# Performance work log

Hardware: AMD Instinct MI355X
Metric: run time of the kernel (lower is better)

Reference implementation:

```python
import jax, jax.numpy as jnp
import numpy as np
import math

N_AGENTS = 16

def _mlp2(x, W1, b1, W2, b2):
    # tanh on first layer only, matching the torch module
    return jnp.tanh(x @ W1 + b1) @ W2 + b2

def setup_inputs() -> dict:
    key = jax.random.key(0)
    ks = jax.random.split(key, 24)
    B, N, A, IN, D = 2048, N_AGENTS, 32, 128, 128
    NODES = B * N
    s = 0.05
    inp = {
        "obs": jax.random.normal(ks[0], (NODES, IN), jnp.float32),
        "policies": jax.random.uniform(ks[1], (NODES, A), jnp.float32),
        "actions": jax.random.uniform(ks[2], (NODES, A), jnp.float32),
        "weights": jax.random.uniform(ks[3], (1,), jnp.float32),
        "noise": jax.random.normal(ks[4], (NODES, N, A), jnp.float32) * 0.1,
        "Wk1": jax.random.normal(ks[5], (IN, 32), jnp.float32) * s,
        "bk1": jnp.zeros((32,), jnp.float32),
        "Wk2": jax.random.normal(ks[6], (32, D), jnp.float32) * s,
        "bk2": jnp.zeros((D,), jnp.float32),
        "Wq1": jax.random.normal(ks[7], (IN, 32), jnp.float32) * s,
        "bq1": jnp.zeros((32,), jnp.float32),
        "Wq2": jax.random.normal(ks[8], (32, D), jnp.float32) * s,
        "bq2": jnp.zeros((D,), jnp.float32),
        "Wv1": jax.random.normal(ks[9], (IN, 32), jnp.float32) * s,
        "bv1": jnp.zeros((32,), jnp.float32),
        "Wv2": jax.random.normal(ks[10], (32, D), jnp.float32) * s,
        "bv2": jnp.zeros((D,), jnp.float32),
        "Wval": jax.random.normal(ks[11], (D + A, 1), jnp.float32) * s,
        "bval": jnp.zeros((1,), jnp.float32),
    }
    return inp

def reference(obs, policies, actions, weights, noise,
              Wk1, bk1, Wk2, bk2, Wq1, bq1, Wq2, bq2, Wv1, bv1, Wv2, bv2,
              Wval, bval):
    N = N_AGENTS
    NODES, _ = obs.shape
    B = NODES // N
    A = policies.shape[-1]
    D = Wk2.shape[1]

    # ---- SoftAttentionInput: graph soft attention over complete N-agent graphs
    k = _mlp2(obs, Wk1, bk1, Wk2, bk2).reshape(B, N, D)
    q = _mlp2(obs, Wq1, bq1, Wq2, bq2).reshape(B, N, D)
    v = _mlp2(obs, Wv1, bv1, Wv2, bv2).reshape(B, N, D)
    # score for receiver i from sender j: key[j] . query[i]
    scores = jnp.einsum('bjd,bid->bij', k, q) / math.sqrt(D)
    alpha = jax.nn.softmax(scores, axis=-1)               # softmax over senders j
    obs_proc = jnp.einsum('bij,bjd->bid', alpha, v)       # [B,N,D]

    # ---- SoftAttentionWeight: PRD mixing of policies and noisy actions
    pi = policies.reshape(B, N, A)
    act = actions.reshape(B, N, A)
    w = weights                                           # scalar mixing weight, shape (1,)
    # z[b,i,k] = w*act[b,k] + (1-w)*pi[b,k] + noise (mailbox of receiver i)
    z = w * act[:, None, :, :] + (1.0 - w) * pi[:, None, :, :] + noise.reshape(B, N, N, A)
    # place_policies construction: z_final[b,i,j,k] = pi[b,k] if k==j else z[b,i,k];
    # mean over k  =>  (pi[b,j] - z[b,i,j] + sum_k z[b,i,k]) / N
    z_sum = jnp.sum(z, axis=2)                            # [B,N,A]
    z_mix = (pi[:, None, :, :] - z + z_sum[:, :, None, :]) / N  # [B,i,j,A]

    obs_b = jnp.broadcast_to(obs_proc[:, None, :, :], (B, N, N, D))  # [b,i,j] = obs_proc[b,j]
    obs_final = jnp.concatenate([obs_b, z_mix], axis=-1).reshape(B * N, N, D + A)

    # ---- ValueNetwork
    x = obs_final @ Wval + bval                           # [B*N, N, 1]
    weights_preproc = alpha.reshape(B * N, N, 1)
    return x, weights_preproc
```

## Files before the change

### kernel.cpp

```cpp
#include <hip/hip_runtime.h>

typedef __attribute__((ext_vector_type(8))) short bf16x8;
typedef __attribute__((ext_vector_type(4))) float f32x4;

__device__ __forceinline__ unsigned short f2bf(float f){
  union { float f; unsigned int u; } v; v.f = f;
  unsigned int u = v.u;
  return (unsigned short)((u + 0x7FFFu + ((u >> 16) & 1u)) >> 16);
}

__device__ __forceinline__ float fast_tanh(float x){
  x = fminf(15.f, fmaxf(-15.f, x));
  float e = __expf(2.f * x);
  return (e - 1.f) / (e + 1.f);
}

__device__ __forceinline__ float dot128(const float* __restrict__ a,
                                        const float* __restrict__ b){
  float s = 0.f;
  for (int c = 0; c < 128; c += 4){
    float4 x = *(const float4*)(a + c);
    float4 y = *(const float4*)(b + c);
    s += x.x*y.x + x.y*y.y + x.z*y.z + x.w*y.w;
  }
  return s;
}

#define GRPSUM(x) { x += __shfl_xor(x, 1); x += __shfl_xor(x, 2); \
                    x += __shfl_xor(x, 4); x += __shfl_xor(x, 8); }


__global__ __launch_bounds__(256) void kn_kernel(
    const float* __restrict__ policies, const float* __restrict__ actions,
    const float* __restrict__ noise, const float* __restrict__ weights,
    const float* __restrict__ Wval, const float* __restrict__ bval,
    const float* __restrict__ Wk1, const float* __restrict__ Wq1, const float* __restrict__ Wv1,
    const float* __restrict__ Wk2, const float* __restrict__ bk2,
    const float* __restrict__ Wq2, const float* __restrict__ bq2,
    const float* __restrict__ Wv2, const float* __restrict__ bv2,
    float* __restrict__ ws, float* __restrict__ out_x)
{
  const int t = threadIdx.x;

  if ((int)blockIdx.x < 4){
    const int tid2 = blockIdx.x * 256 + t;
    const float rs = 0.08838834764831845f;
    unsigned short* bp = (unsigned short*)ws;
    unsigned short* b2 = (unsigned short*)(ws + 6144);

    for (int d = tid2; d < 1602; d += 1024){
      if (d < 1536){
        const int e = d & 7, l = (d >> 3) & 63, tt = d >> 9;
        const int g = (l >> 4) * 8 + e;
        float val = 0.f;
        if (tt < 2){
          const int h = (l & 15) + tt * 16;
          val = rs * dot128(Wk2 + h * 128, Wq2 + g * 128);
        } else if ((l & 15) == 0){
          val = rs * dot128(Wq2 + g * 128, bk2);
        }
        b2[d] = f2bf(val);
      } else if (d < 1600){
        const int h = d - 1536;
        if (h < 32) ws[6912 + h] = rs * dot128(Wk2 + h * 128, bq2);
        else        ws[6944 + (h - 32)] = dot128(Wv2 + (h - 32) * 128, Wval);
      } else if (d == 1600){
        ws[6976] = rs * dot128(bk2, bq2);
      } else {
        ws[6977] = dot128(bv2, Wval);
      }
    }
    for (int idx = tid2; idx < 12288; idx += 1024){
      const int e  = idx & 7;
      const int l  = (idx >> 3) & 63;
      const int kc = (idx >> 9) & 3;
      const int nt = (idx >> 11) & 1;
      const int m  = idx >> 12;
      const float* W1 = (m == 0) ? Wk1 : ((m == 1) ? Wq1 : Wv1);
      const int krow = kc * 32 + (l >> 4) * 8 + e;
      const int col  = nt * 16 + (l & 15);
      bp[idx] = f2bf(W1[krow * 32 + col]);
    }
    return;
  }

  __shared__ __align__(16) float nvw[256];
  __shared__ __align__(16) float pvl[16], avl[16];

  const int b = blockIdx.x - 4;
  const int w = t >> 6, l = t & 63;
  const int q8 = l & 7, r8 = l >> 3;
  const float4 wv4 = *(const float4*)(Wval + 128 + q8 * 4);

  float4 pA0, pA1, aA0, aA1, wpa, wpb;
  const int jp = l >> 2, seg = l & 3;
  if (w == 0){
    const float* pp = policies + (size_t)(b * 16 + jp) * 32 + seg * 8;
    const float* ap = actions  + (size_t)(b * 16 + jp) * 32 + seg * 8;
    pA0 = *(const float4*)(pp);
    pA1 = *(const float4*)(pp + 4);
    aA0 = *(const float4*)(ap);
    aA1 = *(const float4*)(ap + 4);
    wpa = *(const float4*)(Wval + 128 + seg * 8);
    wpb = *(const float4*)(Wval + 132 + seg * 8);
  }

  const float* nbl = noise + (size_t)b * 8192 + (w * 64 + r8) * 32 + q8 * 4;
  float4 nz[8];
#pragma unroll
  for (int p = 0; p < 8; p++) nz[p] = *(const float4*)(nbl + p * 256);
#pragma unroll
  for (int p = 0; p < 8; p++){
    float s = nz[p].x*wv4.x + nz[p].y*wv4.y + nz[p].z*wv4.z + nz[p].w*wv4.w;
    s += __shfl_xor(s, 1); s += __shfl_xor(s, 2); s += __shfl_xor(s, 4);
    if (q8 == 0) nvw[w * 64 + p * 8 + r8] = s;
  }

  if (w == 0){
    float pvv = pA0.x*wpa.x + pA0.y*wpa.y + pA0.z*wpa.z + pA0.w*wpa.w
              + pA1.x*wpb.x + pA1.y*wpb.y + pA1.z*wpb.z + pA1.w*wpb.w;
    float avv = aA0.x*wpa.x + aA0.y*wpa.y + aA0.z*wpa.z + aA0.w*wpa.w
              + aA1.x*wpb.x + aA1.y*wpb.y + aA1.z*wpb.z + aA1.w*wpb.w;
    pvv += __shfl_xor(pvv, 1); pvv += __shfl_xor(pvv, 2);
    avv += __shfl_xor(avv, 1); avv += __shfl_xor(avv, 2);
    if (seg == 0){ pvl[jp] = pvv; avl[jp] = avv; }
  }

  __syncthreads();

  if (w == 0){
    const float wscal = weights[0];
    const float bvs = bval[0];
    const int i = l >> 2, j0 = (l & 3) * 4;
    float4 pv4 = *(const float4*)&pvl[j0];
    float4 av4 = *(const float4*)&avl[j0];
    float4 nv4 = *(const float4*)&nvw[i * 16 + j0];
    const float om = 1.f - wscal;
    float z0 = wscal * av4.x + om * pv4.x + nv4.x;
    float z1 = wscal * av4.y + om * pv4.y + nv4.y;
    float z2 = wscal * av4.z + om * pv4.z + nv4.z;
    float z3 = wscal * av4.w + om * pv4.w + nv4.w;
    float zs = z0 + z1 + z2 + z3;
    zs += __shfl_xor(zs, 1); zs += __shfl_xor(zs, 2);
    float4 o;
    o.x = (pv4.x - z0 + zs) * 0.0625f + bvs;
    o.y = (pv4.y - z1 + zs) * 0.0625f + bvs;
    o.z = (pv4.z - z2 + zs) * 0.0625f + bvs;
    o.w = (pv4.w - z3 + zs) * 0.0625f + bvs;
    *(float4*)(out_x + (size_t)b * 256 + l * 4) = o;
  }
}

__global__ __launch_bounds__(256) void ka_kernel(
    const float* __restrict__ obs,
    const float* __restrict__ bk1p, const float* __restrict__ bq1p, const float* __restrict__ bv1p,
    const float* __restrict__ ws,
    float* __restrict__ out_x, float* __restrict__ out_alpha)
{
  __shared__ __align__(16) unsigned short hk_s[4][512];
  __shared__ __align__(16) unsigned short hq_s[4][512];
  __shared__ __align__(16) unsigned short tq_s[4][512];
  __shared__ __align__(16) float rql_s[4][16];
  __shared__ __align__(16) float vvl_s[4][16];
  __shared__ __align__(16) float ovl_s[4][16];

  const int t = threadIdx.x;
  const int wid = t >> 6, l = t & 63;
  const int b = blockIdx.x * 4 + wid;
  const int li = l & 15, gp = l >> 4;

  const float* orow = obs + (size_t)(b * 16 + li) * 128 + gp * 8;
  float4 ob[8];
#pragma unroll
  for (int kc = 0; kc < 4; kc++){
    ob[kc * 2]     = *(const float4*)(orow + kc * 32);
    ob[kc * 2 + 1] = *(const float4*)(orow + kc * 32 + 4);
  }
  float4 x4 = *(const float4*)(out_x + (size_t)b * 256 + l * 4);

  const bf16x8* bp  = (const bf16x8*)ws;
  const bf16x8* b2p = (const bf16x8*)(ws + 6144);
  const bf16x8 b20 = b2p[l], b21 = b2p[64 + l], b22 = b2p[128 + l];
  const float u0 = ws[6912 + li], u1 = ws[6928 + li];
  const float wv0 = ws[6944 + li], wv1 = ws[6960 + li];
  const float ccv = ws[6976], cvv = ws[6977];
  const float bk0 = bk1p[li], bk1v = bk1p[16 + li];
  const float bq0 = bq1p[li], bq1v = bq1p[16 + li];
  const float bv0 = bv1p[li], bv1v = bv1p[16 + li];

  bf16x8 afr[4];
#pragma unroll
  for (int kc = 0; kc < 4; kc++){
    bf16x8 a;
    a[0]=(short)f2bf(ob[kc*2].x); a[1]=(short)f2bf(ob[kc*2].y);
    a[2]=(short)f2bf(ob[kc*2].z); a[3]=(short)f2bf(ob[kc*2].w);
    a[4]=(short)f2bf(ob[kc*2+1].x); a[5]=(short)f2bf(ob[kc*2+1].y);
    a[6]=(short)f2bf(ob[kc*2+1].z); a[7]=(short)f2bf(ob[kc*2+1].w);
    afr[kc] = a;
  }
  f32x4 acc[6];
#pragma unroll
  for (int mt = 0; mt < 6; mt++){ f32x4 z = {0.f,0.f,0.f,0.f}; acc[mt] = z; }
#pragma unroll
  for (int mt = 0; mt < 6; mt++){
#pragma unroll
    for (int kc = 0; kc < 4; kc++)
      acc[mt] = __builtin_amdgcn_mfma_f32_16x16x32_bf16(afr[kc], bp[(mt*4+kc)*64 + l], acc[mt], 0, 0, 0);
  }

  unsigned short* hkb = hk_s[wid];
  unsigned short* hqb = hq_s[wid];
#pragma unroll
  for (int tile = 0; tile < 2; tile++){
    const float bk_ = tile ? bk1v : bk0;
    const float bq_ = tile ? bq1v : bq0;
    f32x4 ck = acc[tile], cq = acc[2 + tile];
#pragma unroll
    for (int r = 0; r < 4; r++){
      hkb[(gp*4+r)*32 + tile*16 + li] = f2bf(fast_tanh(ck[r] + bk_));
      hqb[(gp*4+r)*32 + tile*16 + li] = f2bf(fast_tanh(cq[r] + bq_));
    }
  }

  {
    f32x4 c0 = acc[4], c1 = acc[5];
    float vp0 = wv0*fast_tanh(c0[0]+bv0) + wv1*fast_tanh(c1[0]+bv1v);
    float vp1 = wv0*fast_tanh(c0[1]+bv0) + wv1*fast_tanh(c1[1]+bv1v);
    float vp2 = wv0*fast_tanh(c0[2]+bv0) + wv1*fast_tanh(c1[2]+bv1v);
    float vp3 = wv0*fast_tanh(c0[3]+bv0) + wv1*fast_tanh(c1[3]+bv1v);
    GRPSUM(vp0); GRPSUM(vp1); GRPSUM(vp2); GRPSUM(vp3);
    if (li == 0){
      float4 vq; vq.x = vp0+cvv; vq.y = vp1+cvv; vq.z = vp2+cvv; vq.w = vp3+cvv;
      *(float4*)&vvl_s[wid][gp*4] = vq;
    }
  }

  const bf16x8 aq = *(const bf16x8*)(hqb + li*32 + gp*8);
  f32x4 cu0 = {u0,u0,u0,u0}, cu1 = {u1,u1,u1,u1}, cu2 = {ccv,ccv,ccv,ccv};
  f32x4 tq0 = __builtin_amdgcn_mfma_f32_16x16x32_bf16(aq, b20, cu0, 0, 0, 0);
  f32x4 tq1 = __builtin_amdgcn_mfma_f32_16x16x32_bf16(aq, b21, cu1, 0, 0, 0);
  f32x4 rqt = __builtin_amdgcn_mfma_f32_16x16x32_bf16(aq, b22, cu2, 0, 0, 0);
  if (li == 0){
    float4 rv; rv.x = rqt[0]; rv.y = rqt[1]; rv.z = rqt[2]; rv.w = rqt[3];
    *(float4*)&rql_s[wid][gp*4] = rv;
  }
  unsigned short* tqb = tq_s[wid];
#pragma unroll
  for (int r = 0; r < 4; r++){
    tqb[(gp*4+r)*32 + li]      = f2bf(tq0[r]);
    tqb[(gp*4+r)*32 + 16 + li] = f2bf(tq1[r]);
  }

  const bf16x8 ak = *(const bf16x8*)(hkb + li*32 + gp*8);
  const bf16x8 bt = *(const bf16x8*)(tqb + li*32 + gp*8);
  f32x4 zz = {0.f,0.f,0.f,0.f};
  f32x4 S = __builtin_amdgcn_mfma_f32_16x16x32_bf16(ak, bt, zz, 0, 0, 0);
  const float rc = rql_s[wid][li];
  float s0 = S[0]+rc, s1 = S[1]+rc, s2 = S[2]+rc, s3 = S[3]+rc;

  float mx = fmaxf(fmaxf(s0, s1), fmaxf(s2, s3));
  mx = fmaxf(mx, __shfl_xor(mx, 16)); mx = fmaxf(mx, __shfl_xor(mx, 32));
  float e0 = __expf(s0-mx), e1 = __expf(s1-mx), e2 = __expf(s2-mx), e3 = __expf(s3-mx);
  float sm = e0+e1+e2+e3;
  sm += __shfl_xor(sm, 16); sm += __shfl_xor(sm, 32);
  const float inv = 1.f / sm;
  const float a0 = e0*inv, a1 = e1*inv, a2 = e2*inv, a3 = e3*inv;

  float* aT = (float*)tqb;
  { float4 av4; av4.x = a0; av4.y = a1; av4.z = a2; av4.w = a3;
    *(float4*)&aT[li*16 + gp*4] = av4; }
  { float4 o4 = *(const float4*)&aT[l*4];
    *(float4*)(out_alpha + (size_t)b*256 + l*4) = o4; }

  float4 vq4 = *(const float4*)&vvl_s[wid][gp*4];
  float ovp = a0*vq4.x + a1*vq4.y + a2*vq4.z + a3*vq4.w;
  ovp += __shfl_xor(ovp, 16); ovp += __shfl_xor(ovp, 32);
  if (l < 16) ovl_s[wid][l] = ovp;

  {
    float4 ov4 = *(const float4*)&ovl_s[wid][(l & 3) * 4];
    x4.x += ov4.x; x4.y += ov4.y; x4.z += ov4.z; x4.w += ov4.w;
    *(float4*)(out_x + (size_t)b * 256 + l * 4) = x4;
  }
}

extern "C" void kernel_launch(void* const* d_in, const int* in_sizes, int n_in,
                              void* d_out, int out_size, void* d_ws, size_t ws_size,
                              hipStream_t stream)
{
  const float* obs      = (const float*)d_in[0];
  const float* policies = (const float*)d_in[1];
  const float* actions  = (const float*)d_in[2];
  const float* weights  = (const float*)d_in[3];
  const float* noise    = (const float*)d_in[4];
  const float* Wk1  = (const float*)d_in[5];
  const float* bk1  = (const float*)d_in[6];
  const float* Wk2  = (const float*)d_in[7];
  const float* bk2  = (const float*)d_in[8];
  const float* Wq1  = (const float*)d_in[9];
  const float* bq1  = (const float*)d_in[10];
  const float* Wq2  = (const float*)d_in[11];
  const float* bq2  = (const float*)d_in[12];
  const float* Wv1  = (const float*)d_in[13];
  const float* bv1  = (const float*)d_in[14];
  const float* Wv2  = (const float*)d_in[15];
  const float* bv2  = (const float*)d_in[16];
  const float* Wval = (const float*)d_in[17];
  const float* bval = (const float*)d_in[18];

  float* out = (float*)d_out;
  float* ws  = (float*)d_ws;

  const int NODES = in_sizes[0] / 128;
  const int B = NODES / 16;

  float* out_x     = out;
  float* out_alpha = out + (size_t)NODES * 16;

  hipLaunchKernelGGL(kn_kernel, dim3(B + 4), dim3(256), 0, stream,
                     policies, actions, noise, weights, Wval, bval,
                     Wk1, Wq1, Wv1, Wk2, bk2, Wq2, bq2, Wv2, bv2,
                     ws, out_x);
  hipLaunchKernelGGL(ka_kernel, dim3(B / 4), dim3(256), 0, stream,
                     obs, bk1, bq1, bv1, ws, out_x, out_alpha);
}
```

Baseline: 29.22 us.

## Split weight prep into tiny kernel and fuse attention and noise paths via atomics

Weight preprocessing moves into a small 64-block kernel that also zero-fills out_x. The noise/policy value path and the attention path then run as different block ranges of one combined launch, each adding its part into out_x with atomicAdd. This removes the dependency where the attention kernel had to read the noise kernel's out_x, so the two memory-heavy stages can overlap. The cost is an extra zero-fill pass over out_x and scalar float atomics in place of vector stores, and the summation order becomes nondeterministic.

```diff
diff --git a/kernel.cpp b/kernel.cpp
--- a/kernel.cpp
+++ b/kernel.cpp
@@ -30,257 +30,264 @@
                     x += __shfl_xor(x, 4); x += __shfl_xor(x, 8); }
 
 
-__global__ __launch_bounds__(256) void kn_kernel(
-    const float* __restrict__ policies, const float* __restrict__ actions,
-    const float* __restrict__ noise, const float* __restrict__ weights,
-    const float* __restrict__ Wval, const float* __restrict__ bval,
+__global__ __launch_bounds__(64) void k0_kernel(
     const float* __restrict__ Wk1, const float* __restrict__ Wq1, const float* __restrict__ Wv1,
     const float* __restrict__ Wk2, const float* __restrict__ bk2,
     const float* __restrict__ Wq2, const float* __restrict__ bq2,
     const float* __restrict__ Wv2, const float* __restrict__ bv2,
-    float* __restrict__ ws, float* __restrict__ out_x)
+    const float* __restrict__ Wval, float* __restrict__ ws,
+    float* __restrict__ out_x, int nx4)
+{
+  const int tid = blockIdx.x * 64 + threadIdx.x;
+  const float rs = 0.08838834764831845f;
+  unsigned short* bp = (unsigned short*)ws;
+  unsigned short* b2 = (unsigned short*)(ws + 6144);
+
+  if (tid < 1536){
+    const int e = tid & 7, l = (tid >> 3) & 63, tt = tid >> 9;
+    const int g = (l >> 4) * 8 + e;
+    float val = 0.f;
+    if (tt < 2){
+      const int h = (l & 15) + tt * 16;
+      val = rs * dot128(Wk2 + h * 128, Wq2 + g * 128);
+    } else if ((l & 15) == 0){
+      val = rs * dot128(Wq2 + g * 128, bk2);
+    }
+    b2[tid] = f2bf(val);
+  } else if (tid < 1600){
+    const int h = tid - 1536;
+    if (h < 32) ws[6912 + h] = rs * dot128(Wk2 + h * 128, bq2);
+    else        ws[6944 + (h - 32)] = dot128(Wv2 + (h - 32) * 128, Wval);
+  } else if (tid == 1600){
+    ws[6976] = rs * dot128(bk2, bq2);
+  } else if (tid == 1601){
+    ws[6977] = dot128(bv2, Wval);
+  }
+
+  for (int idx = tid; idx < 12288; idx += 4096){
+    const int e  = idx & 7;
+    const int l  = (idx >> 3) & 63;
+    const int kc = (idx >> 9) & 3;
+    const int nt = (idx >> 11) & 1;
+    const int m  = idx >> 12;
+    const float* W1 = (m == 0) ? Wk1 : ((m == 1) ? Wq1 : Wv1);
+    const int krow = kc * 32 + (l >> 4) * 8 + e;
+    const int col  = nt * 16 + (l & 15);
+    bp[idx] = f2bf(W1[krow * 32 + col]);
+  }
+
+  float4 z4 = {0.f, 0.f, 0.f, 0.f};
+  float4* ox = (float4*)out_x;
+  for (int i = tid; i < nx4; i += 4096) ox[i] = z4;
+}
+
+__global__ __launch_bounds__(256) void mega_kernel(
+    const float* __restrict__ obs,
+    const float* __restrict__ policies, const float* __restrict__ actions,
+    const float* __restrict__ noise, const float* __restrict__ weights,
+    const float* __restrict__ bk1p, const float* __restrict__ bq1p, const float* __restrict__ bv1p,
+    const float* __restrict__ Wval, const float* __restrict__ bval,
+    const float* __restrict__ ws,
+    float* __restrict__ out_x, float* __restrict__ out_alpha, int BA)
 {
   const int t = threadIdx.x;
-
-  if ((int)blockIdx.x < 4){
-    const int tid2 = blockIdx.x * 256 + t;
-    const float rs = 0.08838834764831845f;
-    unsigned short* bp = (unsigned short*)ws;
-    unsigned short* b2 = (unsigned short*)(ws + 6144);
-
-    for (int d = tid2; d < 1602; d += 1024){
-      if (d < 1536){
-        const int e = d & 7, l = (d >> 3) & 63, tt = d >> 9;
-        const int g = (l >> 4) * 8 + e;
-        float val = 0.f;
-        if (tt < 2){
-          const int h = (l & 15) + tt * 16;
-          val = rs * dot128(Wk2 + h * 128, Wq2 + g * 128);
-        } else if ((l & 15) == 0){
-          val = rs * dot128(Wq2 + g * 128, bk2);
-        }
-        b2[d] = f2bf(val);
-      } else if (d < 1600){
-        const int h = d - 1536;
-        if (h < 32) ws[6912 + h] = rs * dot128(Wk2 + h * 128, bq2);
-        else        ws[6944 + (h - 32)] = dot128(Wv2 + (h - 32) * 128, Wval);
-      } else if (d == 1600){
-        ws[6976] = rs * dot128(bk2, bq2);
-      } else {
-        ws[6977] = dot128(bv2, Wval);
+  const int bid = blockIdx.x;
+
+  if (bid < BA){
+    __shared__ __align__(16) unsigned short hk_s[4][512];
+    __shared__ __align__(16) unsigned short hq_s[4][512];
+    __shared__ __align__(16) unsigned short tq_s[4][512];
+    __shared__ __align__(16) float rql_s[4][16];
+    __shared__ __align__(16) float vvl_s[4][16];
+    __shared__ __align__(16) float ovl_s[4][16];
+
+    const int wid = t >> 6, l = t & 63;
+    const int b = bid * 4 + wid;
+    const int li = l & 15, gp = l >> 4;
+
+    const float* orow = obs + (size_t)(b * 16 + li) * 128 + gp * 8;
+    float4 ob[8];
+#pragma unroll
+    for (int kc = 0; kc < 4; kc++){
+      ob[kc * 2]     = *(const float4*)(orow + kc * 32);
+      ob[kc * 2 + 1] = *(const float4*)(orow + kc * 32 + 4);
+    }
+
+    const bf16x8* bp  = (const bf16x8*)ws;
+    const bf16x8* b2p = (const bf16x8*)(ws + 6144);
+    const bf16x8 b20 = b2p[l], b21 = b2p[64 + l], b22 = b2p[128 + l];
+    const float u0 = ws[6912 + li], u1 = ws[6928 + li];
+    const float wv0 = ws[6944 + li], wv1 = ws[6960 + li];
+    const float ccv = ws[6976], cvv = ws[6977];
+    const float bk0 = bk1p[li], bk1v = bk1p[16 + li];
+    const float bq0 = bq1p[li], bq1v = bq1p[16 + li];
+    const float bv0 = bv1p[li], bv1v = bv1p[16 + li];
+
+    bf16x8 afr[4];
+#pragma unroll
+    for (int kc = 0; kc < 4; kc++){
+      bf16x8 a;
+      a[0]=(short)f2bf(ob[kc*2].x); a[1]=(short)f2bf(ob[kc*2].y);
+      a[2]=(short)f2bf(ob[kc*2].z); a[3]=(short)f2bf(ob[kc*2].w);
+      a[4]=(short)f2bf(ob[kc*2+1].x); a[5]=(short)f2bf(ob[kc*2+1].y);
+      a[6]=(short)f2bf(ob[kc*2+1].z); a[7]=(short)f2bf(ob[kc*2+1].w);
+      afr[kc] = a;
+    }
+    f32x4 acc[6];
+#pragma unroll
+    for (int mt = 0; mt < 6; mt++){ f32x4 z = {0.f,0.f,0.f,0.f}; acc[mt] = z; }
+#pragma unroll
+    for (int mt = 0; mt < 6; mt++){
+#pragma unroll
+      for (int kc = 0; kc < 4; kc++)
+        acc[mt] = __builtin_amdgcn_mfma_f32_16x16x32_bf16(afr[kc], bp[(mt*4+kc)*64 + l], acc[mt], 0, 0, 0);
+    }
+
+    unsigned short* hkb = hk_s[wid];
+    unsigned short* hqb = hq_s[wid];
+#pragma unroll
+    for (int tile = 0; tile < 2; tile++){
+      const float bk_ = tile ? bk1v : bk0;
+      const float bq_ = tile ? bq1v : bq0;
+      f32x4 ck = acc[tile], cq = acc[2 + tile];
+#pragma unroll
+      for (int r = 0; r < 4; r++){
+        hkb[(gp*4+r)*32 + tile*16 + li] = f2bf(fast_tanh(ck[r] + bk_));
+        hqb[(gp*4+r)*32 + tile*16 + li] = f2bf(fast_tanh(cq[r] + bq_));
       }
     }
-    for (int idx = tid2; idx < 12288; idx += 1024){
-      const int e  = idx & 7;
-      const int l  = (idx >> 3) & 63;
-      const int kc = (idx >> 9) & 3;
-      const int nt = (idx >> 11) & 1;
-      const int m  = idx >> 12;
-      const float* W1 = (m == 0) ? Wk1 : ((m == 1) ? Wq1 : Wv1);
-      const int krow = kc * 32 + (l >> 4) * 8 + e;
-      const int col  = nt * 16 + (l & 15);
-      bp[idx] = f2bf(W1[krow * 32 + col]);
+
+    {
+      f32x4 c0 = acc[4], c1 = acc[5];
+      float vp0 = wv0*fast_tanh(c0[0]+bv0) + wv1*fast_tanh(c1[0]+bv1v);
+      float vp1 = wv0*fast_tanh(c0[1]+bv0) + wv1*fast_tanh(c1[1]+bv1v);
+      float vp2 = wv0*fast_tanh(c0[2]+bv0) + wv1*fast_tanh(c1[2]+bv1v);
+      float vp3 = wv0*fast_tanh(c0[3]+bv0) + wv1*fast_tanh(c1[3]+bv1v);
+      GRPSUM(vp0); GRPSUM(vp1); GRPSUM(vp2); GRPSUM(vp3);
+      if (li == 0){
+        float4 vq; vq.x = vp0+cvv; vq.y = vp1+cvv; vq.z = vp2+cvv; vq.w = vp3+cvv;
+        *(float4*)&vvl_s[wid][gp*4] = vq;
+      }
+    }
+
+    const bf16x8 aq = *(const bf16x8*)(hqb + li*32 + gp*8);
+    f32x4 cu0 = {u0,u0,u0,u0}, cu1 = {u1,u1,u1,u1}, cu2 = {ccv,ccv,ccv,ccv};
+    f32x4 tq0 = __builtin_amdgcn_mfma_f32_16x16x32_bf16(aq, b20, cu0, 0, 0, 0);
+    f32x4 tq1 = __builtin_amdgcn_mfma_f32_16x16x32_bf16(aq, b21, cu1, 0, 0, 0);
+    f32x4 rqt = __builtin_amdgcn_mfma_f32_16x16x32_bf16(aq, b22, cu2, 0, 0, 0);
+    if (li == 0){
+      float4 rv; rv.x = rqt[0]; rv.y = rqt[1]; rv.z = rqt[2]; rv.w = rqt[3];
+      *(float4*)&rql_s[wid][gp*4] = rv;
+    }
+    unsigned short* tqb = tq_s[wid];
+#pragma unroll
+    for (int r = 0; r < 4; r++){
+      tqb[(gp*4+r)*32 + li]      = f2bf(tq0[r]);
+      tqb[(gp*4+r)*32 + 16 + li] = f2bf(tq1[r]);
+    }
+
+    const bf16x8 ak = *(const bf16x8*)(hkb + li*32 + gp*8);
+    const bf16x8 bt = *(const bf16x8*)(tqb + li*32 + gp*8);
+    f32x4 zz = {0.f,0.f,0.f,0.f};
+    f32x4 S = __builtin_amdgcn_mfma_f32_16x16x32_bf16(ak, bt, zz, 0, 0, 0);
+    const float rc = rql_s[wid][li];
+    float s0 = S[0]+rc, s1 = S[1]+rc, s2 = S[2]+rc, s3 = S[3]+rc;
+
+    float mx = fmaxf(fmaxf(s0, s1), fmaxf(s2, s3));
+    mx = fmaxf(mx, __shfl_xor(mx, 16)); mx = fmaxf(mx, __shfl_xor(mx, 32));
+    float e0 = __expf(s0-mx), e1 = __expf(s1-mx), e2 = __expf(s2-mx), e3 = __expf(s3-mx);
+    float sm = e0+e1+e2+e3;
+    sm += __shfl_xor(sm, 16); sm += __shfl_xor(sm, 32);
+    const float inv = 1.f / sm;
+    const float a0 = e0*inv, a1 = e1*inv, a2 = e2*inv, a3 = e3*inv;
+
+    float* aT = (float*)tqb;
+    { float4 av4; av4.x = a0; av4.y = a1; av4.z = a2; av4.w = a3;
+      *(float4*)&aT[li*16 + gp*4] = av4; }
+    { float4 o4 = *(const float4*)&aT[l*4];
+      *(float4*)(out_alpha + (size_t)b*256 + l*4) = o4; }
+
+    float4 vq4 = *(const float4*)&vvl_s[wid][gp*4];
+    float ovp = a0*vq4.x + a1*vq4.y + a2*vq4.z + a3*vq4.w;
+    ovp += __shfl_xor(ovp, 16); ovp += __shfl_xor(ovp, 32);
+    if (l < 16) ovl_s[wid][l] = ovp;
+
+    {
+      float4 ov4 = *(const float4*)&ovl_s[wid][(l & 3) * 4];
+      float* dst = out_x + (size_t)b * 256 + l * 4;
+      atomicAdd(dst + 0, ov4.x);
+      atomicAdd(dst + 1, ov4.y);
+      atomicAdd(dst + 2, ov4.z);
+      atomicAdd(dst + 3, ov4.w);
     }
     return;
   }
 
-  __shared__ __align__(16) float nvw[256];
-  __shared__ __align__(16) float pvl[16], avl[16];
-
-  const int b = blockIdx.x - 4;
-  const int w = t >> 6, l = t & 63;
-  const int q8 = l & 7, r8 = l >> 3;
-  const float4 wv4 = *(const float4*)(Wval + 128 + q8 * 4);
-
-  float4 pA0, pA1, aA0, aA1, wpa, wpb;
-  const int jp = l >> 2, seg = l & 3;
-  if (w == 0){
-    const float* pp = policies + (size_t)(b * 16 + jp) * 32 + seg * 8;
-    const float* ap = actions  + (size_t)(b * 16 + jp) * 32 + seg * 8;
-    pA0 = *(const float4*)(pp);
-    pA1 = *(const float4*)(pp + 4);
-    aA0 = *(const float4*)(ap);
-    aA1 = *(const float4*)(ap + 4);
-    wpa = *(const float4*)(Wval + 128 + seg * 8);
-    wpb = *(const float4*)(Wval + 132 + seg * 8);
-  }
-
-  const float* nbl = noise + (size_t)b * 8192 + (w * 64 + r8) * 32 + q8 * 4;
-  float4 nz[8];
-#pragma unroll
-  for (int p = 0; p < 8; p++) nz[p] = *(const float4*)(nbl + p * 256);
-#pragma unroll
-  for (int p = 0; p < 8; p++){
-    float s = nz[p].x*wv4.x + nz[p].y*wv4.y + nz[p].z*wv4.z + nz[p].w*wv4.w;
-    s += __shfl_xor(s, 1); s += __shfl_xor(s, 2); s += __shfl_xor(s, 4);
-    if (q8 == 0) nvw[w * 64 + p * 8 + r8] = s;
-  }
-
-  if (w == 0){
-    float pvv = pA0.x*wpa.x + pA0.y*wpa.y + pA0.z*wpa.z + pA0.w*wpa.w
-              + pA1.x*wpb.x + pA1.y*wpb.y + pA1.z*wpb.z + pA1.w*wpb.w;
-    float avv = aA0.x*wpa.x + aA0.y*wpa.y + aA0.z*wpa.z + aA0.w*wpa.w
-              + aA1.x*wpb.x + aA1.y*wpb.y + aA1.z*wpb.z + aA1.w*wpb.w;
-    pvv += __shfl_xor(pvv, 1); pvv += __shfl_xor(pvv, 2);
-    avv += __shfl_xor(avv, 1); avv += __shfl_xor(avv, 2);
-    if (seg == 0){ pvl[jp] = pvv; avl[jp] = avv; }
-  }
-
-  __syncthreads();
-
-  if (w == 0){
-    const float wscal = weights[0];
-    const float bvs = bval[0];
-    const int i = l >> 2, j0 = (l & 3) * 4;
-    float4 pv4 = *(const float4*)&pvl[j0];
-    float4 av4 = *(const float4*)&avl[j0];
-    float4 nv4 = *(const float4*)&nvw[i * 16 + j0];
-    const float om = 1.f - wscal;
-    float z0 = wscal * av4.x + om * pv4.x + nv4.x;
-    float z1 = wscal * av4.y + om * pv4.y + nv4.y;
-    float z2 = wscal * av4.z + om * pv4.z + nv4.z;
-    float z3 = wscal * av4.w + om * pv4.w + nv4.w;
-    float zs = z0 + z1 + z2 + z3;
-    zs += __shfl_xor(zs, 1); zs += __shfl_xor(zs, 2);
-    float4 o;
-    o.x = (pv4.x - z0 + zs) * 0.0625f + bvs;
-    o.y = (pv4.y - z1 + zs) * 0.0625f + bvs;
-    o.z = (pv4.z - z2 + zs) * 0.0625f + bvs;
-    o.w = (pv4.w - z3 + zs) * 0.0625f + bvs;
-    *(float4*)(out_x + (size_t)b * 256 + l * 4) = o;
-  }
-}
-
-__global__ __launch_bounds__(256) void ka_kernel(
-    const float* __restrict__ obs,
-    const float* __restrict__ bk1p, const float* __restrict__ bq1p, const float* __restrict__ bv1p,
-    const float* __restrict__ ws,
-    float* __restrict__ out_x, float* __restrict__ out_alpha)
-{
-  __shared__ __align__(16) unsigned short hk_s[4][512];
-  __shared__ __align__(16) unsigned short hq_s[4][512];
-  __shared__ __align__(16) unsigned short tq_s[4][512];
-  __shared__ __align__(16) float rql_s[4][16];
-  __shared__ __align__(16) float vvl_s[4][16];
-  __shared__ __align__(16) float ovl_s[4][16];
-
-  const int t = threadIdx.x;
-  const int wid = t >> 6, l = t & 63;
-  const int b = blockIdx.x * 4 + wid;
-  const int li = l & 15, gp = l >> 4;
-
-  const float* orow = obs + (size_t)(b * 16 + li) * 128 + gp * 8;
-  float4 ob[8];
-#pragma unroll
-  for (int kc = 0; kc < 4; kc++){
-    ob[kc * 2]     = *(const float4*)(orow + kc * 32);
-    ob[kc * 2 + 1] = *(const float4*)(orow + kc * 32 + 4);
-  }
-  float4 x4 = *(const float4*)(out_x + (size_t)b * 256 + l * 4);
-
-  const bf16x8* bp  = (const bf16x8*)ws;
-  const bf16x8* b2p = (const bf16x8*)(ws + 6144);
-  const bf16x8 b20 = b2p[l], b21 = b2p[64 + l], b22 = b2p[128 + l];
-  const float u0 = ws[6912 + li], u1 = ws[6928 + li];
-  const float wv0 = ws[6944 + li], wv1 = ws[6960 + li];
-  const float ccv = ws[6976], cvv = ws[6977];
-  const float bk0 = bk1p[li], bk1v = bk1p[16 + li];
-  const float bq0 = bq1p[li], bq1v = bq1p[16 + li];
-  const float bv0 = bv1p[li], bv1v = bv1p[16 + li];
-
-  bf16x8 afr[4];
-#pragma unroll
-  for (int kc = 0; kc < 4; kc++){
-    bf16x8 a;
-    a[0]=(short)f2bf(ob[kc*2].x); a[1]=(short)f2bf(ob[kc*2].y);
-    a[2]=(short)f2bf(ob[kc*2].z); a[3]=(short)f2bf(ob[kc*2].w);
-    a[4]=(short)f2bf(ob[kc*2+1].x); a[5]=(short)f2bf(ob[kc*2+1].y);
-    a[6]=(short)f2bf(ob[kc*2+1].z); a[7]=(short)f2bf(ob[kc*2+1].w);
-    afr[kc] = a;
-  }
-  f32x4 acc[6];
-#pragma unroll
-  for (int mt = 0; mt < 6; mt++){ f32x4 z = {0.f,0.f,0.f,0.f}; acc[mt] = z; }
-#pragma unroll
-  for (int mt = 0; mt < 6; mt++){
-#pragma unroll
-    for (int kc = 0; kc < 4; kc++)
-      acc[mt] = __builtin_amdgcn_mfma_f32_16x16x32_bf16(afr[kc], bp[(mt*4+kc)*64 + l], acc[mt], 0, 0, 0);
-  }
-
-  unsigned short* hkb = hk_s[wid];
-  unsigned short* hqb = hq_s[wid];
-#pragma unroll
-  for (int tile = 0; tile < 2; tile++){
-    const float bk_ = tile ? bk1v : bk0;
-    const float bq_ = tile ? bq1v : bq0;
-    f32x4 ck = acc[tile], cq = acc[2 + tile];
-#pragma unroll
-    for (int r = 0; r < 4; r++){
-      hkb[(gp*4+r)*32 + tile*16 + li] = f2bf(fast_tanh(ck[r] + bk_));
-      hqb[(gp*4+r)*32 + tile*16 + li] = f2bf(fast_tanh(cq[r] + bq_));
-    }
-  }
-
   {
-    f32x4 c0 = acc[4], c1 = acc[5];
-    float vp0 = wv0*fast_tanh(c0[0]+bv0) + wv1*fast_tanh(c1[0]+bv1v);
-    float vp1 = wv0*fast_tanh(c0[1]+bv0) + wv1*fast_tanh(c1[1]+bv1v);
-    float vp2 = wv0*fast_tanh(c0[2]+bv0) + wv1*fast_tanh(c1[2]+bv1v);
-    float vp3 = wv0*fast_tanh(c0[3]+bv0) + wv1*fast_tanh(c1[3]+bv1v);
-    GRPSUM(vp0); GRPSUM(vp1); GRPSUM(vp2); GRPSUM(vp3);
-    if (li == 0){
-      float4 vq; vq.x = vp0+cvv; vq.y = vp1+cvv; vq.z = vp2+cvv; vq.w = vp3+cvv;
-      *(float4*)&vvl_s[wid][gp*4] = vq;
-    }
-  }
-
-  const bf16x8 aq = *(const bf16x8*)(hqb + li*32 + gp*8);
-  f32x4 cu0 = {u0,u0,u0,u0}, cu1 = {u1,u1,u1,u1}, cu2 = {ccv,ccv,ccv,ccv};
-  f32x4 tq0 = __builtin_amdgcn_mfma_f32_16x16x32_bf16(aq, b20, cu0, 0, 0, 0);
-  f32x4 tq1 = __builtin_amdgcn_mfma_f32_16x16x32_bf16(aq, b21, cu1, 0, 0, 0);
-  f32x4 rqt = __builtin_amdgcn_mfma_f32_16x16x32_bf16(aq, b22, cu2, 0, 0, 0);
-  if (li == 0){
-    float4 rv; rv.x = rqt[0]; rv.y = rqt[1]; rv.z = rqt[2]; rv.w = rqt[3];
-    *(float4*)&rql_s[wid][gp*4] = rv;
-  }
-  unsigned short* tqb = tq_s[wid];
-#pragma unroll
-  for (int r = 0; r < 4; r++){
-    tqb[(gp*4+r)*32 + li]      = f2bf(tq0[r]);
-    tqb[(gp*4+r)*32 + 16 + li] = f2bf(tq1[r]);
-  }
-
-  const bf16x8 ak = *(const bf16x8*)(hkb + li*32 + gp*8);
-  const bf16x8 bt = *(const bf16x8*)(tqb + li*32 + gp*8);
-  f32x4 zz = {0.f,0.f,0.f,0.f};
-  f32x4 S = __builtin_amdgcn_mfma_f32_16x16x32_bf16(ak, bt, zz, 0, 0, 0);
-  const float rc = rql_s[wid][li];
-  float s0 = S[0]+rc, s1 = S[1]+rc, s2 = S[2]+rc, s3 = S[3]+rc;
-
-  float mx = fmaxf(fmaxf(s0, s1), fmaxf(s2, s3));
-  mx = fmaxf(mx, __shfl_xor(mx, 16)); mx = fmaxf(mx, __shfl_xor(mx, 32));
-  float e0 = __expf(s0-mx), e1 = __expf(s1-mx), e2 = __expf(s2-mx), e3 = __expf(s3-mx);
-  float sm = e0+e1+e2+e3;
-  sm += __shfl_xor(sm, 16); sm += __shfl_xor(sm, 32);
-  const float inv = 1.f / sm;
-  const float a0 = e0*inv, a1 = e1*inv, a2 = e2*inv, a3 = e3*inv;
-
-  float* aT = (float*)tqb;
-  { float4 av4; av4.x = a0; av4.y = a1; av4.z = a2; av4.w = a3;
-    *(float4*)&aT[li*16 + gp*4] = av4; }
-  { float4 o4 = *(const float4*)&aT[l*4];
-    *(float4*)(out_alpha + (size_t)b*256 + l*4) = o4; }
-
-  float4 vq4 = *(const float4*)&vvl_s[wid][gp*4];
-  float ovp = a0*vq4.x + a1*vq4.y + a2*vq4.z + a3*vq4.w;
-  ovp += __shfl_xor(ovp, 16); ovp += __shfl_xor(ovp, 32);
-  if (l < 16) ovl_s[wid][l] = ovp;
-
-  {
-    float4 ov4 = *(const float4*)&ovl_s[wid][(l & 3) * 4];
-    x4.x += ov4.x; x4.y += ov4.y; x4.z += ov4.z; x4.w += ov4.w;
-    *(float4*)(out_x + (size_t)b * 256 + l * 4) = x4;
+    __shared__ __align__(16) float nvw[256];
+    __shared__ __align__(16) float pvl[16], avl[16];
+
+    const int b = bid - BA;
+    const int w = t >> 6, l = t & 63;
+    const int q8 = l & 7, r8 = l >> 3;
+    const float4 wv4 = *(const float4*)(Wval + 128 + q8 * 4);
+
+    float4 pA0, pA1, aA0, aA1, wpa, wpb;
+    const int jp = l >> 2, seg = l & 3;
+    if (w == 0){
+      const float* pp = policies + (size_t)(b * 16 + jp) * 32 + seg * 8;
+      const float* ap = actions  + (size_t)(b * 16 + jp) * 32 + seg * 8;
+      pA0 = *(const float4*)(pp);
+      pA1 = *(const float4*)(pp + 4);
+      aA0 = *(const float4*)(ap);
+      aA1 = *(const float4*)(ap + 4);
+      wpa = *(const float4*)(Wval + 128 + seg * 8);
+      wpb = *(const float4*)(Wval + 132 + seg * 8);
+    }
+
+    const float* nbl = noise + (size_t)b * 8192 + (w * 64 + r8) * 32 + q8 * 4;
+    float4 nz[8];
+#pragma unroll
+    for (int p = 0; p < 8; p++) nz[p] = *(const float4*)(nbl + p * 256);
+#pragma unroll
+    for (int p = 0; p < 8; p++){
+      float s = nz[p].x*wv4.x + nz[p].y*wv4.y + nz[p].z*wv4.z + nz[p].w*wv4.w;
+      s += __shfl_xor(s, 1); s += __shfl_xor(s, 2); s += __shfl_xor(s, 4);
+      if (q8 == 0) nvw[w * 64 + p * 8 + r8] = s;
+    }
+
+    if (w == 0){
+      float pvv = pA0.x*wpa.x + pA0.y*wpa.y + pA0.z*wpa.z + pA0.w*wpa.w
+                + pA1.x*wpb.x + pA1.y*wpb.y + pA1.z*wpb.z + pA1.w*wpb.w;
+      float avv = aA0.x*wpa.x + aA0.y*wpa.y + aA0.z*wpa.z + aA0.w*wpa.w
+                + aA1.x*wpb.x + aA1.y*wpb.y + aA1.z*wpb.z + aA1.w*wpb.w;
+      pvv += __shfl_xor(pvv, 1); pvv += __shfl_xor(pvv, 2);
+      avv += __shfl_xor(avv, 1); avv += __shfl_xor(avv, 2);
+      if (seg == 0){ pvl[jp] = pvv; avl[jp] = avv; }
+    }
+
+    __syncthreads();
+
+    if (w == 0){
+      const float wscal = weights[0];
+      const float bvs = bval[0];
+      const int i = l >> 2, j0 = (l & 3) * 4;
+      float4 pv4 = *(const float4*)&pvl[j0];
+      float4 av4 = *(const float4*)&avl[j0];
+      float4 nv4 = *(const float4*)&nvw[i * 16 + j0];
+      const float om = 1.f - wscal;
+      float z0 = wscal * av4.x + om * pv4.x + nv4.x;
+      float z1 = wscal * av4.y + om * pv4.y + nv4.y;
+      float z2 = wscal * av4.z + om * pv4.z + nv4.z;
+      float z3 = wscal * av4.w + om * pv4.w + nv4.w;
+      float zs = z0 + z1 + z2 + z3;
+      zs += __shfl_xor(zs, 1); zs += __shfl_xor(zs, 2);
+      float* dst = out_x + (size_t)b * 256 + l * 4;
+      atomicAdd(dst + 0, (pv4.x - z0 + zs) * 0.0625f + bvs);
+      atomicAdd(dst + 1, (pv4.y - z1 + zs) * 0.0625f + bvs);
+      atomicAdd(dst + 2, (pv4.z - z2 + zs) * 0.0625f + bvs);
+      atomicAdd(dst + 3, (pv4.w - z3 + zs) * 0.0625f + bvs);
+    }
   }
 }
 
@@ -313,14 +320,16 @@
 
   const int NODES = in_sizes[0] / 128;
   const int B = NODES / 16;
+  const int BA = B / 4;
 
   float* out_x     = out;
   float* out_alpha = out + (size_t)NODES * 16;
 
-  hipLaunchKernelGGL(kn_kernel, dim3(B + 4), dim3(256), 0, stream,
-                     policies, actions, noise, weights, Wval, bval,
-                     Wk1, Wq1, Wv1, Wk2, bk2, Wq2, bq2, Wv2, bv2,
-                     ws, out_x);
-  hipLaunchKernelGGL(ka_kernel, dim3(B / 4), dim3(256), 0, stream,
-                     obs, bk1, bq1, bv1, ws, out_x, out_alpha);
-}
+  hipLaunchKernelGGL(k0_kernel, dim3(64), dim3(64), 0, stream,
+                     Wk1, Wq1, Wv1, Wk2, bk2, Wq2, bq2, Wv2, bv2, Wval, ws,
+                     out_x, NODES * 16 / 4);
+  hipLaunchKernelGGL(mega_kernel, dim3(BA + B), dim3(256), 0, stream,
+                     obs, policies, actions, noise, weights,
+                     bk1, bq1, bv1, Wval, bval, ws,
+                     out_x, out_alpha, BA);
+}
```

Measured after the change: 36.69 us. +25.6%, slower.

## Recompute packed weights per block in LDS and reorder kernels to drop out_x round-trip

Applied to the files above, without the earlier changes.

Weight preprocessing moves out of kn_kernel's 4 dedicated blocks. It includes the Wk2·Wq2 products, the bias folds and the bf16 packing of the first-layer weights. Every attention block now recomputes them redundantly into shared memory, and the MFMA B-fragments are read from LDS. The launch order is swapped: ka_kernel runs first and writes only the attention-value term to the workspace, then kn_kernel combines it with the mixing term and writes out_x once. This removes the serial dependency on a few prep blocks and the read-modify-write of out_x. The cost is a large amount of duplicated dot-product and packing work in every block, plus extra LDS use.

```diff
diff --git a/kernel.cpp b/kernel.cpp
--- a/kernel.cpp
+++ b/kernel.cpp
@@ -29,145 +29,30 @@
 #define GRPSUM(x) { x += __shfl_xor(x, 1); x += __shfl_xor(x, 2); \
                     x += __shfl_xor(x, 4); x += __shfl_xor(x, 8); }
 
-
-__global__ __launch_bounds__(256) void kn_kernel(
-    const float* __restrict__ policies, const float* __restrict__ actions,
-    const float* __restrict__ noise, const float* __restrict__ weights,
-    const float* __restrict__ Wval, const float* __restrict__ bval,
+__global__ __launch_bounds__(256) void ka_kernel(
+    const float* __restrict__ obs,
     const float* __restrict__ Wk1, const float* __restrict__ Wq1, const float* __restrict__ Wv1,
     const float* __restrict__ Wk2, const float* __restrict__ bk2,
     const float* __restrict__ Wq2, const float* __restrict__ bq2,
     const float* __restrict__ Wv2, const float* __restrict__ bv2,
-    float* __restrict__ ws, float* __restrict__ out_x)
+    const float* __restrict__ Wval,
+    const float* __restrict__ bk1p, const float* __restrict__ bq1p, const float* __restrict__ bv1p,
+    float* __restrict__ out_alpha, float* __restrict__ ws_ov)
 {
-  const int t = threadIdx.x;
-
-  if ((int)blockIdx.x < 4){
-    const int tid2 = blockIdx.x * 256 + t;
-    const float rs = 0.08838834764831845f;
-    unsigned short* bp = (unsigned short*)ws;
-    unsigned short* b2 = (unsigned short*)(ws + 6144);
-
-    for (int d = tid2; d < 1602; d += 1024){
-      if (d < 1536){
-        const int e = d & 7, l = (d >> 3) & 63, tt = d >> 9;
-        const int g = (l >> 4) * 8 + e;
-        float val = 0.f;
-        if (tt < 2){
-          const int h = (l & 15) + tt * 16;
-          val = rs * dot128(Wk2 + h * 128, Wq2 + g * 128);
-        } else if ((l & 15) == 0){
-          val = rs * dot128(Wq2 + g * 128, bk2);
-        }
-        b2[d] = f2bf(val);
-      } else if (d < 1600){
-        const int h = d - 1536;
-        if (h < 32) ws[6912 + h] = rs * dot128(Wk2 + h * 128, bq2);
-        else        ws[6944 + (h - 32)] = dot128(Wv2 + (h - 32) * 128, Wval);
-      } else if (d == 1600){
-        ws[6976] = rs * dot128(bk2, bq2);
-      } else {
-        ws[6977] = dot128(bv2, Wval);
-      }
-    }
-    for (int idx = tid2; idx < 12288; idx += 1024){
-      const int e  = idx & 7;
-      const int l  = (idx >> 3) & 63;
-      const int kc = (idx >> 9) & 3;
-      const int nt = (idx >> 11) & 1;
-      const int m  = idx >> 12;
-      const float* W1 = (m == 0) ? Wk1 : ((m == 1) ? Wq1 : Wv1);
-      const int krow = kc * 32 + (l >> 4) * 8 + e;
-      const int col  = nt * 16 + (l & 15);
-      bp[idx] = f2bf(W1[krow * 32 + col]);
-    }
-    return;
-  }
-
-  __shared__ __align__(16) float nvw[256];
-  __shared__ __align__(16) float pvl[16], avl[16];
-
-  const int b = blockIdx.x - 4;
-  const int w = t >> 6, l = t & 63;
-  const int q8 = l & 7, r8 = l >> 3;
-  const float4 wv4 = *(const float4*)(Wval + 128 + q8 * 4);
-
-  float4 pA0, pA1, aA0, aA1, wpa, wpb;
-  const int jp = l >> 2, seg = l & 3;
-  if (w == 0){
-    const float* pp = policies + (size_t)(b * 16 + jp) * 32 + seg * 8;
-    const float* ap = actions  + (size_t)(b * 16 + jp) * 32 + seg * 8;
-    pA0 = *(const float4*)(pp);
-    pA1 = *(const float4*)(pp + 4);
-    aA0 = *(const float4*)(ap);
-    aA1 = *(const float4*)(ap + 4);
-    wpa = *(const float4*)(Wval + 128 + seg * 8);
-    wpb = *(const float4*)(Wval + 132 + seg * 8);
-  }
-
-  const float* nbl = noise + (size_t)b * 8192 + (w * 64 + r8) * 32 + q8 * 4;
-  float4 nz[8];
-#pragma unroll
-  for (int p = 0; p < 8; p++) nz[p] = *(const float4*)(nbl + p * 256);
-#pragma unroll
-  for (int p = 0; p < 8; p++){
-    float s = nz[p].x*wv4.x + nz[p].y*wv4.y + nz[p].z*wv4.z + nz[p].w*wv4.w;
-    s += __shfl_xor(s, 1); s += __shfl_xor(s, 2); s += __shfl_xor(s, 4);
-    if (q8 == 0) nvw[w * 64 + p * 8 + r8] = s;
-  }
-
-  if (w == 0){
-    float pvv = pA0.x*wpa.x + pA0.y*wpa.y + pA0.z*wpa.z + pA0.w*wpa.w
-              + pA1.x*wpb.x + pA1.y*wpb.y + pA1.z*wpb.z + pA1.w*wpb.w;
-    float avv = aA0.x*wpa.x + aA0.y*wpa.y + aA0.z*wpa.z + aA0.w*wpa.w
-              + aA1.x*wpb.x + aA1.y*wpb.y + aA1.z*wpb.z + aA1.w*wpb.w;
-    pvv += __shfl_xor(pvv, 1); pvv += __shfl_xor(pvv, 2);
-    avv += __shfl_xor(avv, 1); avv += __shfl_xor(avv, 2);
-    if (seg == 0){ pvl[jp] = pvv; avl[jp] = avv; }
-  }
-
-  __syncthreads();
-
-  if (w == 0){
-    const float wscal = weights[0];
-    const float bvs = bval[0];
-    const int i = l >> 2, j0 = (l & 3) * 4;
-    float4 pv4 = *(const float4*)&pvl[j0];
-    float4 av4 = *(const float4*)&avl[j0];
-    float4 nv4 = *(const float4*)&nvw[i * 16 + j0];
-    const float om = 1.f - wscal;
-    float z0 = wscal * av4.x + om * pv4.x + nv4.x;
-    float z1 = wscal * av4.y + om * pv4.y + nv4.y;
-    float z2 = wscal * av4.z + om * pv4.z + nv4.z;
-    float z3 = wscal * av4.w + om * pv4.w + nv4.w;
-    float zs = z0 + z1 + z2 + z3;
-    zs += __shfl_xor(zs, 1); zs += __shfl_xor(zs, 2);
-    float4 o;
-    o.x = (pv4.x - z0 + zs) * 0.0625f + bvs;
-    o.y = (pv4.y - z1 + zs) * 0.0625f + bvs;
-    o.z = (pv4.z - z2 + zs) * 0.0625f + bvs;
-    o.w = (pv4.w - z3 + zs) * 0.0625f + bvs;
-    *(float4*)(out_x + (size_t)b * 256 + l * 4) = o;
-  }
-}
-
-__global__ __launch_bounds__(256) void ka_kernel(
-    const float* __restrict__ obs,
-    const float* __restrict__ bk1p, const float* __restrict__ bq1p, const float* __restrict__ bv1p,
-    const float* __restrict__ ws,
-    float* __restrict__ out_x, float* __restrict__ out_alpha)
-{
+  __shared__ __align__(16) unsigned short bpack_s[12288];
+  __shared__ __align__(16) unsigned short b2_s[1536];
+  __shared__ __align__(16) float u_s[32], wv_s[32], cc_s[2];
   __shared__ __align__(16) unsigned short hk_s[4][512];
   __shared__ __align__(16) unsigned short hq_s[4][512];
   __shared__ __align__(16) unsigned short tq_s[4][512];
   __shared__ __align__(16) float rql_s[4][16];
   __shared__ __align__(16) float vvl_s[4][16];
-  __shared__ __align__(16) float ovl_s[4][16];
 
   const int t = threadIdx.x;
   const int wid = t >> 6, l = t & 63;
   const int b = blockIdx.x * 4 + wid;
   const int li = l & 15, gp = l >> 4;
+  const float rs = 0.08838834764831845f;
 
   const float* orow = obs + (size_t)(b * 16 + li) * 128 + gp * 8;
   float4 ob[8];
@@ -176,14 +61,41 @@
     ob[kc * 2]     = *(const float4*)(orow + kc * 32);
     ob[kc * 2 + 1] = *(const float4*)(orow + kc * 32 + 4);
   }
-  float4 x4 = *(const float4*)(out_x + (size_t)b * 256 + l * 4);
-
-  const bf16x8* bp  = (const bf16x8*)ws;
-  const bf16x8* b2p = (const bf16x8*)(ws + 6144);
-  const bf16x8 b20 = b2p[l], b21 = b2p[64 + l], b22 = b2p[128 + l];
-  const float u0 = ws[6912 + li], u1 = ws[6928 + li];
-  const float wv0 = ws[6944 + li], wv1 = ws[6960 + li];
-  const float ccv = ws[6976], cvv = ws[6977];
+
+  for (int i = t; i < 512; i += 256)
+    if ((i >> 3) & 15) b2_s[1024 + i] = 0;
+  for (int idx = t; idx < 1024; idx += 256){
+    const int h = idx & 31, g = idx >> 5;
+    const float val = rs * dot128(Wk2 + h * 128, Wq2 + g * 128);
+    b2_s[(h >> 4) * 512 + ((((g >> 3) << 4) | (h & 15)) << 3) + (g & 7)] = f2bf(val);
+  }
+  for (int g = t; g < 32; g += 256){
+    const float val = rs * dot128(Wq2 + g * 128, bk2);
+    b2_s[1024 + (g >> 3) * 128 + (g & 7)] = f2bf(val);
+  }
+  for (int idx = t; idx < 66; idx += 256){
+    if (idx < 32)       u_s[idx]       = rs * dot128(Wk2 + idx * 128, bq2);
+    else if (idx < 64)  wv_s[idx - 32] = dot128(Wv2 + (idx - 32) * 128, Wval);
+    else if (idx == 64) cc_s[0]        = rs * dot128(bk2, bq2);
+    else                cc_s[1]        = dot128(bv2, Wval);
+  }
+  for (int idx = t; idx < 12288; idx += 256){
+    const int e  = idx & 7;
+    const int ll = (idx >> 3) & 63;
+    const int kc = (idx >> 9) & 3;
+    const int nt = (idx >> 11) & 1;
+    const int m  = idx >> 12;
+    const float* W1 = (m == 0) ? Wk1 : ((m == 1) ? Wq1 : Wv1);
+    bpack_s[idx] = f2bf(W1[(kc * 32 + (ll >> 4) * 8 + e) * 32 + nt * 16 + (ll & 15)]);
+  }
+  __syncthreads();
+
+  const bf16x8 b20 = *(const bf16x8*)(b2_s + (size_t)l * 8);
+  const bf16x8 b21 = *(const bf16x8*)(b2_s + 512 + (size_t)l * 8);
+  const bf16x8 b22 = *(const bf16x8*)(b2_s + 1024 + (size_t)l * 8);
+  const float u0 = u_s[li], u1 = u_s[16 + li];
+  const float wv0 = wv_s[li], wv1 = wv_s[16 + li];
+  const float ccv = cc_s[0], cvv = cc_s[1];
   const float bk0 = bk1p[li], bk1v = bk1p[16 + li];
   const float bq0 = bq1p[li], bq1v = bq1p[16 + li];
   const float bv0 = bv1p[li], bv1v = bv1p[16 + li];
@@ -204,8 +116,10 @@
 #pragma unroll
   for (int mt = 0; mt < 6; mt++){
 #pragma unroll
-    for (int kc = 0; kc < 4; kc++)
-      acc[mt] = __builtin_amdgcn_mfma_f32_16x16x32_bf16(afr[kc], bp[(mt*4+kc)*64 + l], acc[mt], 0, 0, 0);
+    for (int kc = 0; kc < 4; kc++){
+      const bf16x8 bfr = *(const bf16x8*)(bpack_s + (size_t)((mt*4+kc)*64 + l) * 8);
+      acc[mt] = __builtin_amdgcn_mfma_f32_16x16x32_bf16(afr[kc], bfr, acc[mt], 0, 0, 0);
+    }
   }
 
   unsigned short* hkb = hk_s[wid];
@@ -275,12 +189,69 @@
   float4 vq4 = *(const float4*)&vvl_s[wid][gp*4];
   float ovp = a0*vq4.x + a1*vq4.y + a2*vq4.z + a3*vq4.w;
   ovp += __shfl_xor(ovp, 16); ovp += __shfl_xor(ovp, 32);
-  if (l < 16) ovl_s[wid][l] = ovp;
+  if (l < 16) ws_ov[(size_t)b*16 + l] = ovp;
+}
+
+__global__ __launch_bounds__(256) void kn_kernel(
+    const float* __restrict__ policies, const float* __restrict__ actions,
+    const float* __restrict__ noise, const float* __restrict__ weights,
+    const float* __restrict__ Wval, const float* __restrict__ bval,
+    const float* __restrict__ ws_ov, float* __restrict__ out_x)
+{
+  __shared__ __align__(16) float nvw[256];
+  __shared__ __align__(16) float pvl[16], avl[16], ovl[16];
+
+  const int b = blockIdx.x, t = threadIdx.x;
+  const int w = t >> 6, l = t & 63;
+  const int q8 = l & 7, r8 = l >> 3;
+  const float4 wv4 = *(const float4*)(Wval + 128 + q8 * 4);
+
+  float4 pA0, pA1, aA0, aA1, wpa, wpb;
+  const int jp = l >> 2, seg = l & 3;
+  if (w == 0){
+    if (t < 16) ovl[t] = ws_ov[(size_t)b * 16 + t];
+    const float* pp = policies + (size_t)(b * 16 + jp) * 32 + seg * 8;
+    const float* ap = actions  + (size_t)(b * 16 + jp) * 32 + seg * 8;
+    pA0 = *(const float4*)(pp);
+    pA1 = *(const float4*)(pp + 4);
+    aA0 = *(const float4*)(ap);
+    aA1 = *(const float4*)(ap + 4);
+    wpa = *(const float4*)(Wval + 128 + seg * 8);
+    wpb = *(const float4*)(Wval + 132 + seg * 8);
+  }
+
+  const float* nbl = noise + (size_t)b * 8192 + (w * 64 + r8) * 32 + q8 * 4;
+  float4 nz[8];
+#pragma unroll
+  for (int p = 0; p < 8; p++) nz[p] = *(const float4*)(nbl + p * 256);
+#pragma unroll
+  for (int p = 0; p < 8; p++){
+    float s = nz[p].x*wv4.x + nz[p].y*wv4.y + nz[p].z*wv4.z + nz[p].w*wv4.w;
+    s += __shfl_xor(s, 1); s += __shfl_xor(s, 2); s += __shfl_xor(s, 4);
+    if (q8 == 0) nvw[w * 64 + p * 8 + r8] = s;
+  }
+
+  if (w == 0){
+    float pvv = pA0.x*wpa.x + pA0.y*wpa.y + pA0.z*wpa.z + pA0.w*wpa.w
+              + pA1.x*wpb.x + pA1.y*wpb.y + pA1.z*wpb.z + pA1.w*wpb.w;
+    float avv = aA0.x*wpa.x + aA0.y*wpa.y + aA0.z*wpa.z + aA0.w*wpa.w
+              + aA1.x*wpb.x + aA1.y*wpb.y + aA1.z*wpb.z + aA1.w*wpb.w;
+    pvv += __shfl_xor(pvv, 1); pvv += __shfl_xor(pvv, 2);
+    avv += __shfl_xor(avv, 1); avv += __shfl_xor(avv, 2);
+    if (seg == 0){ pvl[jp] = pvv; avl[jp] = avv; }
+  }
+
+  __syncthreads();
 
   {
-    float4 ov4 = *(const float4*)&ovl_s[wid][(l & 3) * 4];
-    x4.x += ov4.x; x4.y += ov4.y; x4.z += ov4.z; x4.w += ov4.w;
-    *(float4*)(out_x + (size_t)b * 256 + l * 4) = x4;
+    const float wscal = weights[0];
+    const float bvs = bval[0];
+    const int j = t & 15;
+    const float pv = pvl[j], av = avl[j];
+    const float zval = wscal * av + (1.f - wscal) * pv + nvw[t];
+    float zs = zval;
+    GRPSUM(zs);
+    out_x[(size_t)b * 256 + t] = ovl[j] + (pv - zval + zs) * 0.0625f + bvs;
   }
 }
 
@@ -310,6 +281,7 @@
 
   float* out = (float*)d_out;
   float* ws  = (float*)d_ws;
+  float* ws_ov = ws;
 
   const int NODES = in_sizes[0] / 128;
   const int B = NODES / 16;
@@ -317,10 +289,10 @@
   float* out_x     = out;
   float* out_alpha = out + (size_t)NODES * 16;
 
-  hipLaunchKernelGGL(kn_kernel, dim3(B + 4), dim3(256), 0, stream,
+  hipLaunchKernelGGL(ka_kernel, dim3(B / 4), dim3(256), 0, stream,
+                     obs, Wk1, Wq1, Wv1, Wk2, bk2, Wq2, bq2, Wv2, bv2, Wval,
+                     bk1, bq1, bv1, out_alpha, ws_ov);
+  hipLaunchKernelGGL(kn_kernel, dim3(B), dim3(256), 0, stream,
                      policies, actions, noise, weights, Wval, bval,
-                     Wk1, Wq1, Wv1, Wk2, bk2, Wq2, bq2, Wv2, bv2,
-                     ws, out_x);
-  hipLaunchKernelGGL(ka_kernel, dim3(B / 4), dim3(256), 0, stream,
-                     obs, bk1, bq1, bv1, ws, out_x, out_alpha);
-}
+                     ws_ov, out_x);
+}
```

After: 71.84 us. 146% more time.

## Stage packed bf16 weight table in LDS and software-pipeline MFMA B loads

Applied to the files above, without the earlier changes.

Each block now cooperatively copies the packed bf16 weight table and small float constants from global memory into shared memory, with a block barrier, instead of having every wave read B fragments straight from global. The MFMA loop then double-buffers the B fragments, loading the next tile's four fragments from LDS while issuing the current tile's MFMAs. This targets repeated global/L2 latency on weight loads. In exchange it adds about 27KB of LDS per block, which may lower occupancy, plus a __syncthreads and a copy cost paid by every block.

```diff
diff --git a/kernel.cpp b/kernel.cpp
--- a/kernel.cpp
+++ b/kernel.cpp
@@ -157,6 +157,8 @@
     const float* __restrict__ ws,
     float* __restrict__ out_x, float* __restrict__ out_alpha)
 {
+  __shared__ __align__(16) unsigned short tabu[13824];
+  __shared__ __align__(16) float tabf[68];
   __shared__ __align__(16) unsigned short hk_s[4][512];
   __shared__ __align__(16) unsigned short hq_s[4][512];
   __shared__ __align__(16) unsigned short tq_s[4][512];
@@ -178,12 +180,24 @@
   }
   float4 x4 = *(const float4*)(out_x + (size_t)b * 256 + l * 4);
 
-  const bf16x8* bp  = (const bf16x8*)ws;
-  const bf16x8* b2p = (const bf16x8*)(ws + 6144);
+  {
+    const float4* src = (const float4*)ws;
+    float4* dst = (float4*)tabu;
+#pragma unroll
+    for (int i = 0; i < 7; i++){
+      const int idx = t + i * 256;
+      if (idx < 1728) dst[idx] = src[idx];
+    }
+    if (t < 66) tabf[t] = ws[6912 + t];
+  }
+  __syncthreads();
+
+  const bf16x8* bpl = (const bf16x8*)tabu;
+  const bf16x8* b2p = (const bf16x8*)(tabu + 12288);
   const bf16x8 b20 = b2p[l], b21 = b2p[64 + l], b22 = b2p[128 + l];
-  const float u0 = ws[6912 + li], u1 = ws[6928 + li];
-  const float wv0 = ws[6944 + li], wv1 = ws[6960 + li];
-  const float ccv = ws[6976], cvv = ws[6977];
+  const float u0 = tabf[li], u1 = tabf[16 + li];
+  const float wv0 = tabf[32 + li], wv1 = tabf[48 + li];
+  const float ccv = tabf[64], cvv = tabf[65];
   const float bk0 = bk1p[li], bk1v = bk1p[16 + li];
   const float bq0 = bq1p[li], bq1v = bq1p[16 + li];
   const float bv0 = bv1p[li], bv1v = bv1p[16 + li];
@@ -198,14 +212,23 @@
     a[6]=(short)f2bf(ob[kc*2+1].z); a[7]=(short)f2bf(ob[kc*2+1].w);
     afr[kc] = a;
   }
+
   f32x4 acc[6];
 #pragma unroll
   for (int mt = 0; mt < 6; mt++){ f32x4 z = {0.f,0.f,0.f,0.f}; acc[mt] = z; }
+  bf16x8 cur0 = bpl[l], cur1 = bpl[64 + l], cur2 = bpl[128 + l], cur3 = bpl[192 + l];
 #pragma unroll
   for (int mt = 0; mt < 6; mt++){
-#pragma unroll
-    for (int kc = 0; kc < 4; kc++)
-      acc[mt] = __builtin_amdgcn_mfma_f32_16x16x32_bf16(afr[kc], bp[(mt*4+kc)*64 + l], acc[mt], 0, 0, 0);
+    bf16x8 nxt0, nxt1, nxt2, nxt3;
+    if (mt < 5){
+      const int base = (mt + 1) * 256 + l;
+      nxt0 = bpl[base]; nxt1 = bpl[base + 64]; nxt2 = bpl[base + 128]; nxt3 = bpl[base + 192];
+    }
+    acc[mt] = __builtin_amdgcn_mfma_f32_16x16x32_bf16(afr[0], cur0, acc[mt], 0, 0, 0);
+    acc[mt] = __builtin_amdgcn_mfma_f32_16x16x32_bf16(afr[1], cur1, acc[mt], 0, 0, 0);
+    acc[mt] = __builtin_amdgcn_mfma_f32_16x16x32_bf16(afr[2], cur2, acc[mt], 0, 0, 0);
+    acc[mt] = __builtin_amdgcn_mfma_f32_16x16x32_bf16(afr[3], cur3, acc[mt], 0, 0, 0);
+    if (mt < 5){ cur0 = nxt0; cur1 = nxt1; cur2 = nxt2; cur3 = nxt3; }
   }
 
   unsigned short* hkb = hk_s[wid];
```

New measurement: 29.69 us. No clear change (+1.6%).
